# Kernel tuning notes

Hardware: AMD Instinct MI355X
Metric: run time of the kernel (lower is better)

## Reference

```python
import jax, jax.numpy as jnp
import numpy as np

B, T, IN_DIM, LATENT, NUM_TOKENS = 8, 2048, 1024, 256, 4096


def setup_inputs() -> dict:
    key = jax.random.key(0)
    k1, k2, k3 = jax.random.split(key, 3)
    x = jax.random.normal(k1, (B, T, IN_DIM), dtype=jnp.float32)
    # Linear projection params (Kaiming-ish scale)
    W = jax.random.normal(k2, (IN_DIM, LATENT), dtype=jnp.float32) / np.sqrt(IN_DIM)
    b = jnp.zeros((LATENT,), dtype=jnp.float32)
    # Codebook (nn.Embedding with xavier_uniform init ~ small normal here)
    codebook = jax.random.normal(k3, (NUM_TOKENS, LATENT), dtype=jnp.float32) * 0.05
    return {"x": x, "W": W, "b": b, "codebook": codebook}


def reference(x, W, b, codebook):
    # normalization='none' -> identity; projection: Linear(in_dim, latent_dim)
    h = jnp.einsum("btd,de->bte", x, W) + b              # [B,T,latent]
    flat = h.reshape(-1, h.shape[-1])                     # [N,latent]
    # cdist + argmin: squared distance gives identical argmin as euclidean
    # d2[n,k] = |flat[n]|^2 - 2 flat@cb^T + |cb[k]|^2
    d2 = (jnp.sum(flat * flat, axis=-1, keepdims=True)
          - 2.0 * (flat @ codebook.T)
          + jnp.sum(codebook * codebook, axis=-1))        # [N,num_tokens]
    indices = jnp.argmin(d2, axis=-1)                     # [N]
    codes = codebook[indices].reshape(h.shape)            # gather -> [B,T,latent]
    idx = indices.reshape(x.shape[:-1] + (1,))            # [B,T,1]
    return codes, idx
```

## Files before the change

kernel.cpp:

```cpp
#include <hip/hip_runtime.h>

#define NROWS   16384
#define INDIM   1024
#define KDIM    256
#define NCODES  4096
#define G_ROWS  32
#define V_ROWS  64
#define NSTEP   128

#define VBUF    32768

#define MG_ROWS 64
#define MG_KC   64
#define MG_NCH  (INDIM / MG_KC)
#define XP(p)   ((p) * 8192)
#define WP(p)   (24576 + (p) * 32768)
#define MG_LDS  122880

typedef float f32x4 __attribute__((ext_vector_type(4)));
typedef short short8 __attribute__((ext_vector_type(8)));
typedef unsigned short u16x8 __attribute__((ext_vector_type(8)));
typedef unsigned short u16x4 __attribute__((ext_vector_type(4)));

__device__ inline unsigned short f2bf(float f) {
    unsigned u = __builtin_bit_cast(unsigned, f);
    u = (u + 0x7fffu + ((u >> 16) & 1u)) >> 16;
    return (unsigned short)u;
}
__device__ inline float bf2f(unsigned short h) {
    unsigned u = ((unsigned)h) << 16;
    return __builtin_bit_cast(float, u);
}
__device__ inline f32x4 mfma16(u16x8 a, u16x8 b, f32x4 c) {
    return __builtin_amdgcn_mfma_f32_16x16x32_bf16(
        __builtin_bit_cast(short8, a), __builtin_bit_cast(short8, b), c, 0, 0, 0);
}

__global__ __launch_bounds__(256) void wprep_kernel(const float* __restrict__ W,
                                                    unsigned short* __restrict__ wt_hi,
                                                    unsigned short* __restrict__ wt_md,
                                                    unsigned short* __restrict__ wt_lo) {
    const int t = threadIdx.x;
    const int k = blockIdx.x * 4 + (t >> 6);
    const int c0 = (t & 63) * 4;
    f32x4 v = *(const f32x4*)(W + (size_t)k * KDIM + c0);
    #pragma unroll
    for (int i = 0; i < 4; ++i) {
        const unsigned short h = f2bf(v[i]);
        const float r1 = v[i] - bf2f(h);
        const unsigned short m = f2bf(r1);
        const unsigned short lo = f2bf(r1 - bf2f(m));
        wt_hi[(size_t)(c0 + i) * INDIM + k] = h;
        wt_md[(size_t)(c0 + i) * INDIM + k] = m;
        wt_lo[(size_t)(c0 + i) * INDIM + k] = lo;
    }
}

__global__ __launch_bounds__(256, 1) void gemm_mfma_kernel(const float* __restrict__ x,
                                                           const unsigned short* __restrict__ wt_hi,
                                                           const unsigned short* __restrict__ wt_md,
                                                           const unsigned short* __restrict__ wt_lo,
                                                           const float* __restrict__ bvec,
                                                           float* __restrict__ hbuf) {
    __shared__ __align__(16) char lds[MG_LDS];

    const int t  = threadIdx.x;
    const int w  = t >> 6;
    const int l  = t & 63;
    const int nl = l & 15;
    const int g  = l >> 4;
    const size_t n0 = (size_t)blockIdx.x * MG_ROWS;
    const int lb = l * 16;

    f32x4 acc[4][4];
    #pragma unroll
    for (int a = 0; a < 4; ++a)
        #pragma unroll
        for (int b = 0; b < 4; ++b) acc[a][b] = (f32x4){0.f, 0.f, 0.f, 0.f};

    for (int kc = 0; kc < MG_NCH; ++kc) {
        f32x4 xa[2], xb[2];
        #pragma unroll
        for (int c = 0; c < 2; ++c) {
            const int idx = w * 2 + c;
            const int sX = idx >> 2, rsX = idx & 3;
            const float* p = x + (n0 + rsX * 16 + nl) * INDIM + kc * MG_KC + sX * 32 + g * 8;
            xa[c] = *(const f32x4*)(p);
            xb[c] = *(const f32x4*)(p + 4);
        }
        u16x8 wh[8], wm[8], wl[8];
        #pragma unroll
        for (int ci = 0; ci < 4; ++ci)
            #pragma unroll
            for (int sW = 0; sW < 2; ++sW) {
                const int q = ci * 2 + sW;
                const size_t off = (size_t)((w * 4 + ci) * 16 + nl) * INDIM
                                 + kc * MG_KC + sW * 32 + g * 8;
                wh[q] = *(const u16x8*)(wt_hi + off);
                wm[q] = *(const u16x8*)(wt_md + off);
                wl[q] = *(const u16x8*)(wt_lo + off);
            }
        __syncthreads();

        #pragma unroll
        for (int c = 0; c < 2; ++c) {
            const int idx = w * 2 + c;
            const int sX = idx >> 2, rsX = idx & 3;
            u16x8 xh, xm, xl;
            #pragma unroll
            for (int e = 0; e < 4; ++e) {
                const float a0 = xa[c][e], a1 = xb[c][e];
                const unsigned short h0 = f2bf(a0);
                const float r10 = a0 - bf2f(h0);
                const unsigned short m0 = f2bf(r10);
                const unsigned short l0 = f2bf(r10 - bf2f(m0));
                const unsigned short h1 = f2bf(a1);
                const float r11 = a1 - bf2f(h1);
                const unsigned short m1 = f2bf(r11);
                const unsigned short l1 = f2bf(r11 - bf2f(m1));
                xh[e] = h0; xh[4+e] = h1;
                xm[e] = m0; xm[4+e] = m1;
                xl[e] = l0; xl[4+e] = l1;
            }
            const int base = (sX * 4 + rsX) * 1024 + lb;
            *(u16x8*)(lds + XP(0) + base) = xh;
            *(u16x8*)(lds + XP(1) + base) = xm;
            *(u16x8*)(lds + XP(2) + base) = xl;
        }
        #pragma unroll
        for (int ci = 0; ci < 4; ++ci)
            #pragma unroll
            for (int sW = 0; sW < 2; ++sW) {
                const int q = ci * 2 + sW;
                const int base = (sW * 16 + w * 4 + ci) * 1024 + lb;
                *(u16x8*)(lds + WP(0) + base) = wh[q];
                *(u16x8*)(lds + WP(1) + base) = wm[q];
                *(u16x8*)(lds + WP(2) + base) = wl[q];
            }
        __syncthreads();

        #pragma unroll
        for (int s = 0; s < 2; ++s) {
            u16x8 bh[4], bm[4], bl[4], ah[4], am[4], al[4];
            #pragma unroll
            for (int rs = 0; rs < 4; ++rs) {
                const int base = (s * 4 + rs) * 1024 + lb;
                bh[rs] = *(const u16x8*)(lds + XP(0) + base);
                bm[rs] = *(const u16x8*)(lds + XP(1) + base);
                bl[rs] = *(const u16x8*)(lds + XP(2) + base);
            }
            #pragma unroll
            for (int ct = 0; ct < 4; ++ct) {
                const int base = (s * 16 + w * 4 + ct) * 1024 + lb;
                ah[ct] = *(const u16x8*)(lds + WP(0) + base);
                am[ct] = *(const u16x8*)(lds + WP(1) + base);
                al[ct] = *(const u16x8*)(lds + WP(2) + base);
            }
            #pragma unroll
            for (int ct = 0; ct < 4; ++ct)
                #pragma unroll
                for (int rs = 0; rs < 4; ++rs) {
                    acc[ct][rs] = mfma16(ah[ct], bh[rs], acc[ct][rs]);
                    acc[ct][rs] = mfma16(ah[ct], bm[rs], acc[ct][rs]);
                    acc[ct][rs] = mfma16(am[ct], bh[rs], acc[ct][rs]);
                    acc[ct][rs] = mfma16(ah[ct], bl[rs], acc[ct][rs]);
                    acc[ct][rs] = mfma16(al[ct], bh[rs], acc[ct][rs]);
                    acc[ct][rs] = mfma16(am[ct], bm[rs], acc[ct][rs]);
                }
        }
    }

    #pragma unroll
    for (int ct = 0; ct < 4; ++ct) {
        float bv[4];
        #pragma unroll
        for (int r = 0; r < 4; ++r) bv[r] = bvec[w * 64 + ct * 16 + g * 4 + r];
        #pragma unroll
        for (int rs = 0; rs < 4; ++rs) {
            const size_t row = n0 + rs * 16 + nl;
            #pragma unroll
            for (int r = 0; r < 4; ++r)
                hbuf[row * KDIM + w * 64 + ct * 16 + g * 4 + r] = acc[ct][rs][r] + bv[r];
        }
    }
}

__global__ __launch_bounds__(256, 2) void gemm_fb_kernel(const float* __restrict__ x,
                                                         const float* __restrict__ W,
                                                         const float* __restrict__ bvec,
                                                         float* __restrict__ hbuf) {
    const int t  = threadIdx.x;
    const int cg = t & 15;
    const int rg = t >> 4;
    const size_t n0 = (size_t)blockIdx.x * G_ROWS;
    const int c0 = cg * 16;

    float acc[2][16];
    #pragma unroll
    for (int j = 0; j < 2; ++j)
        #pragma unroll
        for (int cc = 0; cc < 16; ++cc) acc[j][cc] = 0.f;

    for (int k4 = 0; k4 < INDIM / 4; ++k4) {
        const int k = k4 * 4;
        f32x4 xv[2];
        #pragma unroll
        for (int j = 0; j < 2; ++j)
            xv[j] = *(const f32x4*)(x + (n0 + rg + 16 * j) * INDIM + k);
        f32x4 wv[4][4];
        #pragma unroll
        for (int kk = 0; kk < 4; ++kk)
            #pragma unroll
            for (int q = 0; q < 4; ++q)
                wv[kk][q] = *(const f32x4*)(W + (size_t)(k + kk) * KDIM + c0 + 4 * q);
        #pragma unroll
        for (int j = 0; j < 2; ++j)
            #pragma unroll
            for (int kk = 0; kk < 4; ++kk) {
                const float xs = xv[j][kk];
                #pragma unroll
                for (int q = 0; q < 4; ++q)
                    #pragma unroll
                    for (int e = 0; e < 4; ++e)
                        acc[j][4*q+e] = fmaf(xs, wv[kk][q][e], acc[j][4*q+e]);
            }
    }
    #pragma unroll
    for (int j = 0; j < 2; ++j) {
        float* dst = hbuf + (n0 + rg + 16 * j) * KDIM + c0;
        #pragma unroll
        for (int q = 0; q < 4; ++q) {
            f32x4 v;
            #pragma unroll
            for (int e = 0; e < 4; ++e) v[e] = acc[j][4*q+e] + bvec[c0 + 4*q + e];
            *(f32x4*)(dst + 4*q) = v;
        }
    }
}

__global__ __launch_bounds__(256) void prep_kernel(const float* __restrict__ cb,
                                                   float* __restrict__ cnorm,
                                                   unsigned short* __restrict__ cb_hi,
                                                   unsigned short* __restrict__ cb_lo,
                                                   int do_split) {
    const int c    = blockIdx.x * 4 + (threadIdx.x >> 6);
    const int lane = threadIdx.x & 63;
    f32x4 v = ((const f32x4*)(cb + (size_t)c * KDIM))[lane];
    if (do_split) {
        u16x4 h4, l4;
        #pragma unroll
        for (int j = 0; j < 4; ++j) {
            unsigned short h = f2bf(v[j]);
            h4[j] = h;
            l4[j] = f2bf(v[j] - bf2f(h));
        }
        *(u16x4*)(cb_hi + (size_t)c * KDIM + lane * 4) = h4;
        *(u16x4*)(cb_lo + (size_t)c * KDIM + lane * 4) = l4;
    }
    float s = v[0]*v[0] + v[1]*v[1] + v[2]*v[2] + v[3]*v[3];
    #pragma unroll
    for (int off = 1; off < 64; off <<= 1) s += __shfl_xor(s, off);
    if (lane == 0) cnorm[c] = s;
}

template<int PRE>
__global__ __launch_bounds__(256) void vq_kernel(
    float* __restrict__ hbuf,
    const float* __restrict__ cb,
    const float* __restrict__ cnorm,
    const unsigned short* __restrict__ cb_hi,
    const unsigned short* __restrict__ cb_lo,
    float* __restrict__ idx_out)
{
    __shared__ __align__(16) char lds[2 * VBUF];

    const int t  = threadIdx.x;
    const int w  = t >> 6;
    const int l  = t & 63;
    const int nl = l & 15;
    const int g  = l >> 4;
    const int lb = l * 16;
    const size_t n0 = (size_t)blockIdx.x * V_ROWS;
    const int row = w * 16 + nl;
    float* hrow = hbuf + (n0 + row) * KDIM;

    u16x8 bhi[8], bmid[8];
    #pragma unroll
    for (int s = 0; s < 8; ++s) {
        f32x4 a = *(const f32x4*)(hrow + s * 32 + g * 8);
        f32x4 b = *(const f32x4*)(hrow + s * 32 + g * 8 + 4);
        u16x8 uh, um;
        #pragma unroll
        for (int jj = 0; jj < 4; ++jj) {
            unsigned short h0 = f2bf(a[jj]); uh[jj]   = h0; um[jj]   = f2bf(a[jj] - bf2f(h0));
            unsigned short h1 = f2bf(b[jj]); uh[4+jj] = h1; um[4+jj] = f2bf(b[jj] - bf2f(h1));
        }
        bhi[s] = uh; bmid[s] = um;
    }

    float v1 = 3.4e38f, v2 = 3.4e38f;
    int   i1 = 0, i2 = 0;

    u16x8 rh[2][2], rl[2][2];

    #pragma unroll
    for (int t2 = 0; t2 < 2; ++t2)
        #pragma unroll
        for (int sv = 0; sv < 2; ++sv) {
            const int sst = w * 2 + sv;
            if (PRE) {
                const size_t off = (size_t)(t2 * 16 + nl) * KDIM + (sst * 4 + g) * 8;
                rh[t2][sv] = *(const u16x8*)(cb_hi + off);
                rl[t2][sv] = *(const u16x8*)(cb_lo + off);
            } else {
                const float* p = cb + (size_t)(t2 * 16 + nl) * KDIM + (sst * 4 + g) * 8;
                f32x4 a = *(const f32x4*)(p);
                f32x4 b = *(const f32x4*)(p + 4);
                u16x8 uh, ul;
                #pragma unroll
                for (int jj = 0; jj < 4; ++jj) {
                    unsigned short h0 = f2bf(a[jj]); uh[jj]   = h0; ul[jj]   = f2bf(a[jj] - bf2f(h0));
                    unsigned short h1 = f2bf(b[jj]); uh[4+jj] = h1; ul[4+jj] = f2bf(b[jj] - bf2f(h1));
                }
                rh[t2][sv] = uh; rl[t2][sv] = ul;
            }
        }
    #pragma unroll
    for (int t2 = 0; t2 < 2; ++t2)
        #pragma unroll
        for (int sv = 0; sv < 2; ++sv) {
            const int base = (t2 * 8 + w * 2 + sv) * 1024 + lb;
            *(u16x8*)(lds + base) = rh[t2][sv];
            *(u16x8*)(lds + 16384 + base) = rl[t2][sv];
        }
    __syncthreads();

    for (int S = 0; S < NSTEP; ++S) {
        const int b = S & 1;
        if (S + 1 < NSTEP) {
            #pragma unroll
            for (int t2 = 0; t2 < 2; ++t2)
                #pragma unroll
                for (int sv = 0; sv < 2; ++sv) {
                    const int sst = w * 2 + sv;
                    const int code = (S + 1) * 32 + t2 * 16 + nl;
                    if (PRE) {
                        const size_t off = (size_t)code * KDIM + (sst * 4 + g) * 8;
                        rh[t2][sv] = *(const u16x8*)(cb_hi + off);
                        rl[t2][sv] = *(const u16x8*)(cb_lo + off);
                    } else {
                        const float* p = cb + (size_t)code * KDIM + (sst * 4 + g) * 8;
                        f32x4 a = *(const f32x4*)(p);
                        f32x4 bb = *(const f32x4*)(p + 4);
                        u16x8 uh, ul;
                        #pragma unroll
                        for (int jj = 0; jj < 4; ++jj) {
                            unsigned short h0 = f2bf(a[jj]);  uh[jj]   = h0; ul[jj]   = f2bf(a[jj] - bf2f(h0));
                            unsigned short h1 = f2bf(bb[jj]); uh[4+jj] = h1; ul[4+jj] = f2bf(bb[jj] - bf2f(h1));
                        }
                        rh[t2][sv] = uh; rl[t2][sv] = ul;
                    }
                }
        }
        f32x4 cn0 = *(const f32x4*)(cnorm + S * 32 + g * 4);
        f32x4 cn1 = *(const f32x4*)(cnorm + S * 32 + 16 + g * 4);
        {
            const char* buf = lds + b * VBUF;
            #pragma unroll
            for (int t2 = 0; t2 < 2; ++t2) {
                f32x4 acc = {0.f, 0.f, 0.f, 0.f};
                #pragma unroll
                for (int s = 0; s < 8; ++s) {
                    const int base = (t2 * 8 + s) * 1024 + lb;
                    u16x8 ahi = *(const u16x8*)(buf + base);
                    u16x8 alo = *(const u16x8*)(buf + 16384 + base);
                    acc = mfma16(ahi, bhi[s],  acc);
                    acc = mfma16(ahi, bmid[s], acc);
                    acc = mfma16(alo, bhi[s],  acc);
                }
                const f32x4 cn = t2 ? cn1 : cn0;
                #pragma unroll
                for (int r = 0; r < 4; ++r) {
                    const float d2 = cn[r] - 2.0f * acc[r];
                    const int c = S * 32 + t2 * 16 + g * 4 + r;
                    if (d2 < v1)      { v2 = v1; i2 = i1; v1 = d2; i1 = c; }
                    else if (d2 < v2) { v2 = d2; i2 = c; }
                }
            }
        }
        __syncthreads();
        if (S + 1 < NSTEP) {
            char* nbuf = lds + (b ^ 1) * VBUF;
            #pragma unroll
            for (int t2 = 0; t2 < 2; ++t2)
                #pragma unroll
                for (int sv = 0; sv < 2; ++sv) {
                    const int base = (t2 * 8 + w * 2 + sv) * 1024 + lb;
                    *(u16x8*)(nbuf + base) = rh[t2][sv];
                    *(u16x8*)(nbuf + 16384 + base) = rl[t2][sv];
                }
        }
        __syncthreads();
    }

    #pragma unroll
    for (int off = 16; off <= 32; off <<= 1) {
        float ov1 = __shfl_xor(v1, off); int oi1 = __shfl_xor(i1, off);
        float ov2 = __shfl_xor(v2, off); int oi2 = __shfl_xor(i2, off);
        if (ov1 < v1 || (ov1 == v1 && oi1 < i1)) {
            float tv = v1; int ti = i1; v1 = ov1; i1 = oi1; ov1 = tv; oi1 = ti;
            tv = v2; ti = i2; v2 = ov2; i2 = oi2; ov2 = tv; oi2 = ti;
        }
        if (ov1 < v2 || (ov1 == v2 && oi1 < i2)) { v2 = ov1; i2 = oi1; }
    }

    i1 = (i1 < 0) ? 0 : (i1 > NCODES - 1 ? NCODES - 1 : i1);
    i2 = (i2 < 0) ? 0 : (i2 > NCODES - 1 ? NCODES - 1 : i2);

    const float* cp1 = cb + (size_t)i1 * KDIM;
    const float* cp2 = cb + (size_t)i2 * KDIM;
    float da = 0.f, db = 0.f;
    #pragma unroll
    for (int s = 0; s < 8; ++s) {
        f32x4 h0 = *(const f32x4*)(hrow + s * 32 + g * 8);
        f32x4 h1 = *(const f32x4*)(hrow + s * 32 + g * 8 + 4);
        f32x4 a1 = *(const f32x4*)(cp1 + s * 32 + g * 8);
        f32x4 b1 = *(const f32x4*)(cp1 + s * 32 + g * 8 + 4);
        f32x4 a2 = *(const f32x4*)(cp2 + s * 32 + g * 8);
        f32x4 b2 = *(const f32x4*)(cp2 + s * 32 + g * 8 + 4);
        #pragma unroll
        for (int jj = 0; jj < 4; ++jj) {
            da = fmaf(a1[jj], h0[jj], da); da = fmaf(b1[jj], h1[jj], da);
            db = fmaf(a2[jj], h0[jj], db); db = fmaf(b2[jj], h1[jj], db);
        }
    }
    da += __shfl_xor(da, 16); da += __shfl_xor(da, 32);
    db += __shfl_xor(db, 16); db += __shfl_xor(db, 32);
    const float d2a = cnorm[i1] - 2.f * da;
    const float d2b = cnorm[i2] - 2.f * db;
    const int win = (d2a < d2b || (d2a == d2b && i1 < i2)) ? i1 : i2;

    const float* cw = cb + (size_t)win * KDIM;
    #pragma unroll
    for (int s = 0; s < 8; ++s) {
        *(f32x4*)(hrow + s * 32 + g * 8)     = *(const f32x4*)(cw + s * 32 + g * 8);
        *(f32x4*)(hrow + s * 32 + g * 8 + 4) = *(const f32x4*)(cw + s * 32 + g * 8 + 4);
    }
    if (g == 0) idx_out[n0 + row] = (float)win;
}

extern "C" void kernel_launch(void* const* d_in, const int* in_sizes, int n_in,
                              void* d_out, int out_size, void* d_ws, size_t ws_size,
                              hipStream_t stream) {
    (void)in_sizes; (void)n_in; (void)out_size;
    const float* x    = (const float*)d_in[0];
    const float* W    = (const float*)d_in[1];
    const float* bvec = (const float*)d_in[2];
    const float* cb   = (const float*)d_in[3];

    float* codes_out = (float*)d_out;
    float* idx_out   = (float*)d_out + (size_t)NROWS * KDIM;

    float* cnorm = (float*)d_ws;
    unsigned short* cb_hi = (unsigned short*)((char*)d_ws + 16384);
    unsigned short* cb_lo = cb_hi + (size_t)NCODES * KDIM;
    unsigned short* wt_hi = cb_lo + (size_t)NCODES * KDIM;
    unsigned short* wt_md = wt_hi + (size_t)INDIM * KDIM;
    unsigned short* wt_lo = wt_md + (size_t)INDIM * KDIM;

    const size_t need_cb   = 16384 + (size_t)NCODES * KDIM * 2 * sizeof(unsigned short);
    const size_t need_full = need_cb + (size_t)INDIM * KDIM * 3 * sizeof(unsigned short);

    const int pre_cb = (ws_size >= need_cb) ? 1 : 0;
    const int fast_g = (ws_size >= need_full) ? 1 : 0;

    if (fast_g) {
        wprep_kernel<<<INDIM / 4, 256, 0, stream>>>(W, wt_hi, wt_md, wt_lo);
        gemm_mfma_kernel<<<NROWS / MG_ROWS, 256, 0, stream>>>(x, wt_hi, wt_md, wt_lo, bvec, codes_out);
    } else {
        gemm_fb_kernel<<<NROWS / G_ROWS, 256, 0, stream>>>(x, W, bvec, codes_out);
    }
    prep_kernel<<<NCODES / 4, 256, 0, stream>>>(cb, cnorm, cb_hi, cb_lo, pre_cb);
    if (pre_cb)
        vq_kernel<1><<<NROWS / V_ROWS, 256, 0, stream>>>(codes_out, cb, cnorm, cb_hi, cb_lo, idx_out);
    else
        vq_kernel<0><<<NROWS / V_ROWS, 256, 0, stream>>>(codes_out, cb, cnorm, cb_hi, cb_lo, idx_out);
}
```

Baseline: 304.2 us.

## Stream codebook tiles directly from global memory, dropping LDS double buffering

The VQ kernel no longer stages codebook hi/lo bf16 tiles through double-buffered shared memory with two block barriers per step. Each wave now loads its codebook fragments straight from global (cache-resident) memory, processes 64 codes per iteration across four independent accumulators, and removes all __syncthreads from the main loop. This trades LDS traffic and barrier stalls for four times more global/L2 load traffic per block, since each wave re-reads the same codebook data instead of sharing it. It also frees LDS, which may raise occupancy.

```diff
diff --git a/kernel.cpp b/kernel.cpp
--- a/kernel.cpp
+++ b/kernel.cpp
@@ -6,9 +6,7 @@
 #define NCODES  4096
 #define G_ROWS  32
 #define V_ROWS  64
-#define NSTEP   128
-
-#define VBUF    32768
+#define VITER   64
 
 #define MG_ROWS 64
 #define MG_KC   64
@@ -272,14 +270,11 @@
     const unsigned short* __restrict__ cb_lo,
     float* __restrict__ idx_out)
 {
-    __shared__ __align__(16) char lds[2 * VBUF];
-
     const int t  = threadIdx.x;
     const int w  = t >> 6;
     const int l  = t & 63;
     const int nl = l & 15;
     const int g  = l >> 4;
-    const int lb = l * 16;
     const size_t n0 = (size_t)blockIdx.x * V_ROWS;
     const int row = w * 16 + nl;
     float* hrow = hbuf + (n0 + row) * KDIM;
@@ -301,106 +296,54 @@
     float v1 = 3.4e38f, v2 = 3.4e38f;
     int   i1 = 0, i2 = 0;
 
-    u16x8 rh[2][2], rl[2][2];
-
-    #pragma unroll
-    for (int t2 = 0; t2 < 2; ++t2)
-        #pragma unroll
-        for (int sv = 0; sv < 2; ++sv) {
-            const int sst = w * 2 + sv;
-            if (PRE) {
-                const size_t off = (size_t)(t2 * 16 + nl) * KDIM + (sst * 4 + g) * 8;
-                rh[t2][sv] = *(const u16x8*)(cb_hi + off);
-                rl[t2][sv] = *(const u16x8*)(cb_lo + off);
-            } else {
-                const float* p = cb + (size_t)(t2 * 16 + nl) * KDIM + (sst * 4 + g) * 8;
-                f32x4 a = *(const f32x4*)(p);
-                f32x4 b = *(const f32x4*)(p + 4);
-                u16x8 uh, ul;
-                #pragma unroll
-                for (int jj = 0; jj < 4; ++jj) {
-                    unsigned short h0 = f2bf(a[jj]); uh[jj]   = h0; ul[jj]   = f2bf(a[jj] - bf2f(h0));
-                    unsigned short h1 = f2bf(b[jj]); uh[4+jj] = h1; ul[4+jj] = f2bf(b[jj] - bf2f(h1));
+    for (int it = 0; it < VITER; ++it) {
+        const int base_c = it * 64;
+        f32x4 cnv[4];
+        #pragma unroll
+        for (int cg = 0; cg < 4; ++cg)
+            cnv[cg] = *(const f32x4*)(cnorm + base_c + cg * 16 + g * 4);
+
+        f32x4 acc[4];
+        #pragma unroll
+        for (int cg = 0; cg < 4; ++cg) acc[cg] = (f32x4){0.f, 0.f, 0.f, 0.f};
+
+        #pragma unroll
+        for (int s = 0; s < 8; ++s) {
+            #pragma unroll
+            for (int cg = 0; cg < 4; ++cg) {
+                const int code = base_c + cg * 16 + nl;
+                u16x8 ahi, alo;
+                if (PRE) {
+                    const size_t off = (size_t)code * KDIM + (s * 4 + g) * 8;
+                    ahi = *(const u16x8*)(cb_hi + off);
+                    alo = *(const u16x8*)(cb_lo + off);
+                } else {
+                    const float* p = cb + (size_t)code * KDIM + (s * 4 + g) * 8;
+                    f32x4 a = *(const f32x4*)(p);
+                    f32x4 b = *(const f32x4*)(p + 4);
+                    u16x8 uh, ul;
+                    #pragma unroll
+                    for (int jj = 0; jj < 4; ++jj) {
+                        unsigned short h0 = f2bf(a[jj]); uh[jj]   = h0; ul[jj]   = f2bf(a[jj] - bf2f(h0));
+                        unsigned short h1 = f2bf(b[jj]); uh[4+jj] = h1; ul[4+jj] = f2bf(b[jj] - bf2f(h1));
+                    }
+                    ahi = uh; alo = ul;
                 }
-                rh[t2][sv] = uh; rl[t2][sv] = ul;
-            }
-        }
-    #pragma unroll
-    for (int t2 = 0; t2 < 2; ++t2)
-        #pragma unroll
-        for (int sv = 0; sv < 2; ++sv) {
-            const int base = (t2 * 8 + w * 2 + sv) * 1024 + lb;
-            *(u16x8*)(lds + base) = rh[t2][sv];
-            *(u16x8*)(lds + 16384 + base) = rl[t2][sv];
-        }
-    __syncthreads();
-
-    for (int S = 0; S < NSTEP; ++S) {
-        const int b = S & 1;
-        if (S + 1 < NSTEP) {
-            #pragma unroll
-            for (int t2 = 0; t2 < 2; ++t2)
-                #pragma unroll
-                for (int sv = 0; sv < 2; ++sv) {
-                    const int sst = w * 2 + sv;
-                    const int code = (S + 1) * 32 + t2 * 16 + nl;
-                    if (PRE) {
-                        const size_t off = (size_t)code * KDIM + (sst * 4 + g) * 8;
-                        rh[t2][sv] = *(const u16x8*)(cb_hi + off);
-                        rl[t2][sv] = *(const u16x8*)(cb_lo + off);
-                    } else {
-                        const float* p = cb + (size_t)code * KDIM + (sst * 4 + g) * 8;
-                        f32x4 a = *(const f32x4*)(p);
-                        f32x4 bb = *(const f32x4*)(p + 4);
-                        u16x8 uh, ul;
-                        #pragma unroll
-                        for (int jj = 0; jj < 4; ++jj) {
-                            unsigned short h0 = f2bf(a[jj]);  uh[jj]   = h0; ul[jj]   = f2bf(a[jj] - bf2f(h0));
-                            unsigned short h1 = f2bf(bb[jj]); uh[4+jj] = h1; ul[4+jj] = f2bf(bb[jj] - bf2f(h1));
-                        }
-                        rh[t2][sv] = uh; rl[t2][sv] = ul;
-                    }
-                }
-        }
-        f32x4 cn0 = *(const f32x4*)(cnorm + S * 32 + g * 4);
-        f32x4 cn1 = *(const f32x4*)(cnorm + S * 32 + 16 + g * 4);
-        {
-            const char* buf = lds + b * VBUF;
-            #pragma unroll
-            for (int t2 = 0; t2 < 2; ++t2) {
-                f32x4 acc = {0.f, 0.f, 0.f, 0.f};
-                #pragma unroll
-                for (int s = 0; s < 8; ++s) {
-                    const int base = (t2 * 8 + s) * 1024 + lb;
-                    u16x8 ahi = *(const u16x8*)(buf + base);
-                    u16x8 alo = *(const u16x8*)(buf + 16384 + base);
-                    acc = mfma16(ahi, bhi[s],  acc);
-                    acc = mfma16(ahi, bmid[s], acc);
-                    acc = mfma16(alo, bhi[s],  acc);
-                }
-                const f32x4 cn = t2 ? cn1 : cn0;
-                #pragma unroll
-                for (int r = 0; r < 4; ++r) {
-                    const float d2 = cn[r] - 2.0f * acc[r];
-                    const int c = S * 32 + t2 * 16 + g * 4 + r;
-                    if (d2 < v1)      { v2 = v1; i2 = i1; v1 = d2; i1 = c; }
-                    else if (d2 < v2) { v2 = d2; i2 = c; }
-                }
-            }
-        }
-        __syncthreads();
-        if (S + 1 < NSTEP) {
-            char* nbuf = lds + (b ^ 1) * VBUF;
-            #pragma unroll
-            for (int t2 = 0; t2 < 2; ++t2)
-                #pragma unroll
-                for (int sv = 0; sv < 2; ++sv) {
-                    const int base = (t2 * 8 + w * 2 + sv) * 1024 + lb;
-                    *(u16x8*)(nbuf + base) = rh[t2][sv];
-                    *(u16x8*)(nbuf + 16384 + base) = rl[t2][sv];
-                }
-        }
-        __syncthreads();
+                acc[cg] = mfma16(ahi, bhi[s],  acc[cg]);
+                acc[cg] = mfma16(ahi, bmid[s], acc[cg]);
+                acc[cg] = mfma16(alo, bhi[s],  acc[cg]);
+            }
+        }
+
+        #pragma unroll
+        for (int cg = 0; cg < 4; ++cg)
+            #pragma unroll
+            for (int r = 0; r < 4; ++r) {
+                const float d2 = cnv[cg][r] - 2.0f * acc[cg][r];
+                const int c = base_c + cg * 16 + g * 4 + r;
+                if (d2 < v1)      { v2 = v1; i2 = i1; v1 = d2; i1 = c; }
+                else if (d2 < v2) { v2 = d2; i2 = c; }
+            }
     }
 
     #pragma unroll
```

New measurement: 803.0 us. +164.0%, slower.

## Split VQ codebook search across two blocks per row tile with merge kernel

Applied to the files above, without the earlier changes.

The nearest-code search now splits the 4096-code scan into two halves handled by separate blocks, doubling the grid from 256 to 512 blocks. Each block writes its top-2 candidates to a workspace record, and a new merge kernel combines the halves, rechecks the two finalists in fp32, gathers the winning code and writes the index. This targets low occupancy, since 256 blocks underfill the GPU's CUs. In exchange it adds an extra launch, a second pass over h, and a workspace reshuffle that shifts the codebook buffers.

```diff
diff --git a/kernel.cpp b/kernel.cpp
--- a/kernel.cpp
+++ b/kernel.cpp
@@ -18,6 +18,7 @@
 #define MG_LDS  122880
 
 typedef float f32x4 __attribute__((ext_vector_type(4)));
+typedef int   i32x4 __attribute__((ext_vector_type(4)));
 typedef short short8 __attribute__((ext_vector_type(8)));
 typedef unsigned short u16x8 __attribute__((ext_vector_type(8)));
 typedef unsigned short u16x4 __attribute__((ext_vector_type(4)));
@@ -264,13 +265,13 @@
 }
 
 template<int PRE>
-__global__ __launch_bounds__(256) void vq_kernel(
-    float* __restrict__ hbuf,
+__global__ __launch_bounds__(256) void vq_partial_kernel(
+    const float* __restrict__ hbuf,
     const float* __restrict__ cb,
     const float* __restrict__ cnorm,
     const unsigned short* __restrict__ cb_hi,
     const unsigned short* __restrict__ cb_lo,
-    float* __restrict__ idx_out)
+    int* __restrict__ recs)
 {
     __shared__ __align__(16) char lds[2 * VBUF];
 
@@ -280,9 +281,12 @@
     const int nl = l & 15;
     const int g  = l >> 4;
     const int lb = l * 16;
-    const size_t n0 = (size_t)blockIdx.x * V_ROWS;
+    const int bid  = blockIdx.x;
+    const int half = bid & 1;
+    const int S0   = half * 64;
+    const size_t n0 = (size_t)(bid >> 1) * V_ROWS;
     const int row = w * 16 + nl;
-    float* hrow = hbuf + (n0 + row) * KDIM;
+    const float* hrow = hbuf + (n0 + row) * KDIM;
 
     u16x8 bhi[8], bmid[8];
     #pragma unroll
@@ -308,12 +312,13 @@
         #pragma unroll
         for (int sv = 0; sv < 2; ++sv) {
             const int sst = w * 2 + sv;
+            const int code = S0 * 32 + t2 * 16 + nl;
             if (PRE) {
-                const size_t off = (size_t)(t2 * 16 + nl) * KDIM + (sst * 4 + g) * 8;
+                const size_t off = (size_t)code * KDIM + (sst * 4 + g) * 8;
                 rh[t2][sv] = *(const u16x8*)(cb_hi + off);
                 rl[t2][sv] = *(const u16x8*)(cb_lo + off);
             } else {
-                const float* p = cb + (size_t)(t2 * 16 + nl) * KDIM + (sst * 4 + g) * 8;
+                const float* p = cb + (size_t)code * KDIM + (sst * 4 + g) * 8;
                 f32x4 a = *(const f32x4*)(p);
                 f32x4 b = *(const f32x4*)(p + 4);
                 u16x8 uh, ul;
@@ -335,9 +340,9 @@
         }
     __syncthreads();
 
-    for (int S = 0; S < NSTEP; ++S) {
+    for (int S = S0; S < S0 + 64; ++S) {
         const int b = S & 1;
-        if (S + 1 < NSTEP) {
+        if (S + 1 < S0 + 64) {
             #pragma unroll
             for (int t2 = 0; t2 < 2; ++t2)
                 #pragma unroll
@@ -389,6 +394,231 @@
             }
         }
         __syncthreads();
+        if (S + 1 < S0 + 64) {
+            char* nbuf = lds + (b ^ 1) * VBUF;
+            #pragma unroll
+            for (int t2 = 0; t2 < 2; ++t2)
+                #pragma unroll
+                for (int sv = 0; sv < 2; ++sv) {
+                    const int base = (t2 * 8 + w * 2 + sv) * 1024 + lb;
+                    *(u16x8*)(nbuf + base) = rh[t2][sv];
+                    *(u16x8*)(nbuf + 16384 + base) = rl[t2][sv];
+                }
+        }
+        __syncthreads();
+    }
+
+    #pragma unroll
+    for (int off = 16; off <= 32; off <<= 1) {
+        float ov1 = __shfl_xor(v1, off); int oi1 = __shfl_xor(i1, off);
+        float ov2 = __shfl_xor(v2, off); int oi2 = __shfl_xor(i2, off);
+        if (ov1 < v1 || (ov1 == v1 && oi1 < i1)) {
+            float tv = v1; int ti = i1; v1 = ov1; i1 = oi1; ov1 = tv; oi1 = ti;
+            tv = v2; ti = i2; v2 = ov2; i2 = oi2; ov2 = tv; oi2 = ti;
+        }
+        if (ov1 < v2 || (ov1 == v2 && oi1 < i2)) { v2 = ov1; i2 = oi1; }
+    }
+
+    if (g == 0) {
+        i32x4 rec;
+        rec[0] = __builtin_bit_cast(int, v1); rec[1] = i1;
+        rec[2] = __builtin_bit_cast(int, v2); rec[3] = i2;
+        *(i32x4*)(recs + (((n0 + row) * 2) + half) * 4) = rec;
+    }
+}
+
+__global__ __launch_bounds__(256) void vq_merge_kernel(
+    float* __restrict__ hbuf,
+    const float* __restrict__ cb,
+    const float* __restrict__ cnorm,
+    const int* __restrict__ recs,
+    float* __restrict__ idx_out)
+{
+    const int t  = threadIdx.x;
+    const int w  = t >> 6;
+    const int l  = t & 63;
+    const int nl = l & 15;
+    const int g  = l >> 4;
+    const size_t n0 = (size_t)blockIdx.x * V_ROWS;
+    const int row = w * 16 + nl;
+    float* hrow = hbuf + (n0 + row) * KDIM;
+
+    const size_t rb = ((n0 + row) * 2) * 4;
+    i32x4 r0 = *(const i32x4*)(recs + rb);
+    i32x4 r1 = *(const i32x4*)(recs + rb + 4);
+    float v1 = __builtin_bit_cast(float, r0[0]); int i1 = r0[1];
+    float v2 = __builtin_bit_cast(float, r0[2]); int i2 = r0[3];
+    {
+        float ov1 = __builtin_bit_cast(float, r1[0]); int oi1 = r1[1];
+        float ov2 = __builtin_bit_cast(float, r1[2]); int oi2 = r1[3];
+        if (ov1 < v1 || (ov1 == v1 && oi1 < i1)) {
+            float tv = v1; int ti = i1; v1 = ov1; i1 = oi1; ov1 = tv; oi1 = ti;
+            tv = v2; ti = i2; v2 = ov2; i2 = oi2; ov2 = tv; oi2 = ti;
+        }
+        if (ov1 < v2 || (ov1 == v2 && oi1 < i2)) { v2 = ov1; i2 = oi1; }
+    }
+
+    i1 = (i1 < 0) ? 0 : (i1 > NCODES - 1 ? NCODES - 1 : i1);
+    i2 = (i2 < 0) ? 0 : (i2 > NCODES - 1 ? NCODES - 1 : i2);
+
+    const float* cp1 = cb + (size_t)i1 * KDIM;
+    const float* cp2 = cb + (size_t)i2 * KDIM;
+    float da = 0.f, db = 0.f;
+    #pragma unroll
+    for (int s = 0; s < 8; ++s) {
+        f32x4 h0 = *(const f32x4*)(hrow + s * 32 + g * 8);
+        f32x4 h1 = *(const f32x4*)(hrow + s * 32 + g * 8 + 4);
+        f32x4 a1 = *(const f32x4*)(cp1 + s * 32 + g * 8);
+        f32x4 b1 = *(const f32x4*)(cp1 + s * 32 + g * 8 + 4);
+        f32x4 a2 = *(const f32x4*)(cp2 + s * 32 + g * 8);
+        f32x4 b2 = *(const f32x4*)(cp2 + s * 32 + g * 8 + 4);
+        #pragma unroll
+        for (int jj = 0; jj < 4; ++jj) {
+            da = fmaf(a1[jj], h0[jj], da); da = fmaf(b1[jj], h1[jj], da);
+            db = fmaf(a2[jj], h0[jj], db); db = fmaf(b2[jj], h1[jj], db);
+        }
+    }
+    da += __shfl_xor(da, 16); da += __shfl_xor(da, 32);
+    db += __shfl_xor(db, 16); db += __shfl_xor(db, 32);
+    const float d2a = cnorm[i1] - 2.f * da;
+    const float d2b = cnorm[i2] - 2.f * db;
+    const int win = (d2a < d2b || (d2a == d2b && i1 < i2)) ? i1 : i2;
+
+    const float* cw = cb + (size_t)win * KDIM;
+    #pragma unroll
+    for (int s = 0; s < 8; ++s) {
+        *(f32x4*)(hrow + s * 32 + g * 8)     = *(const f32x4*)(cw + s * 32 + g * 8);
+        *(f32x4*)(hrow + s * 32 + g * 8 + 4) = *(const f32x4*)(cw + s * 32 + g * 8 + 4);
+    }
+    if (g == 0) idx_out[n0 + row] = (float)win;
+}
+
+template<int PRE>
+__global__ __launch_bounds__(256) void vq_kernel(
+    float* __restrict__ hbuf,
+    const float* __restrict__ cb,
+    const float* __restrict__ cnorm,
+    const unsigned short* __restrict__ cb_hi,
+    const unsigned short* __restrict__ cb_lo,
+    float* __restrict__ idx_out)
+{
+    __shared__ __align__(16) char lds[2 * VBUF];
+
+    const int t  = threadIdx.x;
+    const int w  = t >> 6;
+    const int l  = t & 63;
+    const int nl = l & 15;
+    const int g  = l >> 4;
+    const int lb = l * 16;
+    const size_t n0 = (size_t)blockIdx.x * V_ROWS;
+    const int row = w * 16 + nl;
+    float* hrow = hbuf + (n0 + row) * KDIM;
+
+    u16x8 bhi[8], bmid[8];
+    #pragma unroll
+    for (int s = 0; s < 8; ++s) {
+        f32x4 a = *(const f32x4*)(hrow + s * 32 + g * 8);
+        f32x4 b = *(const f32x4*)(hrow + s * 32 + g * 8 + 4);
+        u16x8 uh, um;
+        #pragma unroll
+        for (int jj = 0; jj < 4; ++jj) {
+            unsigned short h0 = f2bf(a[jj]); uh[jj]   = h0; um[jj]   = f2bf(a[jj] - bf2f(h0));
+            unsigned short h1 = f2bf(b[jj]); uh[4+jj] = h1; um[4+jj] = f2bf(b[jj] - bf2f(h1));
+        }
+        bhi[s] = uh; bmid[s] = um;
+    }
+
+    float v1 = 3.4e38f, v2 = 3.4e38f;
+    int   i1 = 0, i2 = 0;
+
+    u16x8 rh[2][2], rl[2][2];
+
+    #pragma unroll
+    for (int t2 = 0; t2 < 2; ++t2)
+        #pragma unroll
+        for (int sv = 0; sv < 2; ++sv) {
+            const int sst = w * 2 + sv;
+            if (PRE) {
+                const size_t off = (size_t)(t2 * 16 + nl) * KDIM + (sst * 4 + g) * 8;
+                rh[t2][sv] = *(const u16x8*)(cb_hi + off);
+                rl[t2][sv] = *(const u16x8*)(cb_lo + off);
+            } else {
+                const float* p = cb + (size_t)(t2 * 16 + nl) * KDIM + (sst * 4 + g) * 8;
+                f32x4 a = *(const f32x4*)(p);
+                f32x4 b = *(const f32x4*)(p + 4);
+                u16x8 uh, ul;
+                #pragma unroll
+                for (int jj = 0; jj < 4; ++jj) {
+                    unsigned short h0 = f2bf(a[jj]); uh[jj]   = h0; ul[jj]   = f2bf(a[jj] - bf2f(h0));
+                    unsigned short h1 = f2bf(b[jj]); uh[4+jj] = h1; ul[4+jj] = f2bf(b[jj] - bf2f(h1));
+                }
+                rh[t2][sv] = uh; rl[t2][sv] = ul;
+            }
+        }
+    #pragma unroll
+    for (int t2 = 0; t2 < 2; ++t2)
+        #pragma unroll
+        for (int sv = 0; sv < 2; ++sv) {
+            const int base = (t2 * 8 + w * 2 + sv) * 1024 + lb;
+            *(u16x8*)(lds + base) = rh[t2][sv];
+            *(u16x8*)(lds + 16384 + base) = rl[t2][sv];
+        }
+    __syncthreads();
+
+    for (int S = 0; S < NSTEP; ++S) {
+        const int b = S & 1;
+        if (S + 1 < NSTEP) {
+            #pragma unroll
+            for (int t2 = 0; t2 < 2; ++t2)
+                #pragma unroll
+                for (int sv = 0; sv < 2; ++sv) {
+                    const int sst = w * 2 + sv;
+                    const int code = (S + 1) * 32 + t2 * 16 + nl;
+                    if (PRE) {
+                        const size_t off = (size_t)code * KDIM + (sst * 4 + g) * 8;
+                        rh[t2][sv] = *(const u16x8*)(cb_hi + off);
+                        rl[t2][sv] = *(const u16x8*)(cb_lo + off);
+                    } else {
+                        const float* p = cb + (size_t)code * KDIM + (sst * 4 + g) * 8;
+                        f32x4 a = *(const f32x4*)(p);
+                        f32x4 bb = *(const f32x4*)(p + 4);
+                        u16x8 uh, ul;
+                        #pragma unroll
+                        for (int jj = 0; jj < 4; ++jj) {
+                            unsigned short h0 = f2bf(a[jj]);  uh[jj]   = h0; ul[jj]   = f2bf(a[jj] - bf2f(h0));
+                            unsigned short h1 = f2bf(bb[jj]); uh[4+jj] = h1; ul[4+jj] = f2bf(bb[jj] - bf2f(h1));
+                        }
+                        rh[t2][sv] = uh; rl[t2][sv] = ul;
+                    }
+                }
+        }
+        f32x4 cn0 = *(const f32x4*)(cnorm + S * 32 + g * 4);
+        f32x4 cn1 = *(const f32x4*)(cnorm + S * 32 + 16 + g * 4);
+        {
+            const char* buf = lds + b * VBUF;
+            #pragma unroll
+            for (int t2 = 0; t2 < 2; ++t2) {
+                f32x4 acc = {0.f, 0.f, 0.f, 0.f};
+                #pragma unroll
+                for (int s = 0; s < 8; ++s) {
+                    const int base = (t2 * 8 + s) * 1024 + lb;
+                    u16x8 ahi = *(const u16x8*)(buf + base);
+                    u16x8 alo = *(const u16x8*)(buf + 16384 + base);
+                    acc = mfma16(ahi, bhi[s],  acc);
+                    acc = mfma16(ahi, bmid[s], acc);
+                    acc = mfma16(alo, bhi[s],  acc);
+                }
+                const f32x4 cn = t2 ? cn1 : cn0;
+                #pragma unroll
+                for (int r = 0; r < 4; ++r) {
+                    const float d2 = cn[r] - 2.0f * acc[r];
+                    const int c = S * 32 + t2 * 16 + g * 4 + r;
+                    if (d2 < v1)      { v2 = v1; i2 = i1; v1 = d2; i1 = c; }
+                    else if (d2 < v2) { v2 = d2; i2 = c; }
+                }
+            }
+        }
+        __syncthreads();
         if (S + 1 < NSTEP) {
             char* nbuf = lds + (b ^ 1) * VBUF;
             #pragma unroll
@@ -462,17 +692,20 @@
     float* idx_out   = (float*)d_out + (size_t)NROWS * KDIM;
 
     float* cnorm = (float*)d_ws;
-    unsigned short* cb_hi = (unsigned short*)((char*)d_ws + 16384);
+    int*   recs  = (int*)((char*)d_ws + 16384);
+    unsigned short* cb_hi = (unsigned short*)((char*)d_ws + 16384 + 524288);
     unsigned short* cb_lo = cb_hi + (size_t)NCODES * KDIM;
     unsigned short* wt_hi = cb_lo + (size_t)NCODES * KDIM;
     unsigned short* wt_md = wt_hi + (size_t)INDIM * KDIM;
     unsigned short* wt_lo = wt_md + (size_t)INDIM * KDIM;
 
-    const size_t need_cb   = 16384 + (size_t)NCODES * KDIM * 2 * sizeof(unsigned short);
+    const size_t need_rec  = 16384 + 524288;
+    const size_t need_cb   = need_rec + (size_t)NCODES * KDIM * 2 * sizeof(unsigned short);
     const size_t need_full = need_cb + (size_t)INDIM * KDIM * 3 * sizeof(unsigned short);
 
-    const int pre_cb = (ws_size >= need_cb) ? 1 : 0;
-    const int fast_g = (ws_size >= need_full) ? 1 : 0;
+    const int use_split = (ws_size >= need_rec) ? 1 : 0;
+    const int pre_cb    = (ws_size >= need_cb) ? 1 : 0;
+    const int fast_g    = (ws_size >= need_full) ? 1 : 0;
 
     if (fast_g) {
         wprep_kernel<<<INDIM / 4, 256, 0, stream>>>(W, wt_hi, wt_md, wt_lo);
@@ -481,8 +714,17 @@
         gemm_fb_kernel<<<NROWS / G_ROWS, 256, 0, stream>>>(x, W, bvec, codes_out);
     }
     prep_kernel<<<NCODES / 4, 256, 0, stream>>>(cb, cnorm, cb_hi, cb_lo, pre_cb);
-    if (pre_cb)
-        vq_kernel<1><<<NROWS / V_ROWS, 256, 0, stream>>>(codes_out, cb, cnorm, cb_hi, cb_lo, idx_out);
-    else
-        vq_kernel<0><<<NROWS / V_ROWS, 256, 0, stream>>>(codes_out, cb, cnorm, cb_hi, cb_lo, idx_out);
-}
+
+    if (use_split) {
+        if (pre_cb)
+            vq_partial_kernel<1><<<(NROWS / V_ROWS) * 2, 256, 0, stream>>>(codes_out, cb, cnorm, cb_hi, cb_lo, recs);
+        else
+            vq_partial_kernel<0><<<(NROWS / V_ROWS) * 2, 256, 0, stream>>>(codes_out, cb, cnorm, cb_hi, cb_lo, recs);
+        vq_merge_kernel<<<NROWS / V_ROWS, 256, 0, stream>>>(codes_out, cb, cnorm, recs, idx_out);
+    } else {
+        if (pre_cb)
+            vq_kernel<1><<<NROWS / V_ROWS, 256, 0, stream>>>(codes_out, cb, cnorm, cb_hi, cb_lo, idx_out);
+        else
+            vq_kernel<0><<<NROWS / V_ROWS, 256, 0, stream>>>(codes_out, cb, cnorm, cb_hi, cb_lo, idx_out);
+    }
+}
```

Measured after the change: 255.2 us. -16.1%, faster.
